# Performance work log

Measured on AMD Instinct MI355X. Metric: run time of the kernel, lower is better.

Reference implementation:

```python
import jax, jax.numpy as jnp
import numpy as np

N_NODES = 50000
N_EDGES = 400000
D_IN = 2048
D_OUT = 512


def setup_inputs() -> dict:
    key = jax.random.key(0)
    k1, k2, k3 = jax.random.split(key, 3)
    x = jax.random.normal(k1, (N_NODES, D_IN), dtype=jnp.float32)
    edge_index = jax.random.randint(k2, (2, N_EDGES), 0, N_NODES, dtype=jnp.int64)
    # Glorot init like PyG GCNConv
    scale = jnp.sqrt(6.0 / (D_IN + D_OUT)).astype(jnp.float32)
    weight = jax.random.uniform(k3, (D_IN, D_OUT), dtype=jnp.float32, minval=-scale, maxval=scale)
    bias = jnp.zeros((D_OUT,), dtype=jnp.float32)
    return {"x": x, "edge_index": edge_index, "weight": weight, "bias": bias}


def reference(x, edge_index, weight, bias):
    N = x.shape[0]
    # GCNConv(normalize=True): add self-loops, symmetric deg^-1/2 normalization
    loops = jnp.arange(N, dtype=edge_index.dtype)
    src = jnp.concatenate([edge_index[0], loops])  # message sources (x_j)
    dst = jnp.concatenate([edge_index[1], loops])  # aggregation targets
    ones = jnp.ones(dst.shape[0], dtype=x.dtype)
    deg = jax.ops.segment_sum(ones, dst, num_segments=N)  # [N]
    deg_inv_sqrt = jnp.where(deg > 0, jax.lax.rsqrt(deg), 0.0)
    norm = deg_inv_sqrt[src] * deg_inv_sqrt[dst]  # [E+N]
    h = x @ weight  # [N, d_out] linear transform before propagation
    msgs = norm[:, None] * h[src]  # [E+N, d_out]
    out = jax.ops.segment_sum(msgs, dst, num_segments=N) + bias  # [N, d_out]
    return jax.nn.log_softmax(out, axis=1)
```

## Files before the change

kernel.cpp:

```cpp
#include <hip/hip_runtime.h>
#include <stdint.h>

#define D_IN   2048
#define D_OUT  512

typedef __bf16 bf16;
typedef bf16     bf16x8 __attribute__((ext_vector_type(8)));
typedef float    f32x4  __attribute__((ext_vector_type(4)));
typedef uint32_t u32x4  __attribute__((ext_vector_type(4)));

#define GLP(p)  (const __attribute__((address_space(1))) void*)(p)
#define LDSP(p) (__attribute__((address_space(3))) void*)(p)

__global__ void k_count(const int* __restrict__ dstv, int* __restrict__ cnt, int E) {
    int e = blockIdx.x * blockDim.x + threadIdx.x;
    if (e < E) atomicAdd(&cnt[dstv[e]], 1);
}

__global__ __launch_bounds__(1024) void k_scan1(const int* __restrict__ cnt,
                                                int* __restrict__ offs,
                                                int* __restrict__ bsum,
                                                float* __restrict__ dis,
                                                int* __restrict__ cur, int n) {
    __shared__ int wsum[16], wbase[16];
    const int tid = threadIdx.x, lane = tid & 63, wv = tid >> 6;
    int i = blockIdx.x * 1024 + tid;
    int v = (i < n) ? cnt[i] : 0;
    int x = v;
    #pragma unroll
    for (int d = 1; d < 64; d <<= 1) {
        int y = __shfl_up(x, d);
        if (lane >= d) x += y;
    }
    if (lane == 63) wsum[wv] = x;
    __syncthreads();
    if (tid < 16) {
        int s = 0;
        for (int j = 0; j < tid; ++j) s += wsum[j];
        wbase[tid] = s;
    }
    __syncthreads();
    if (i < n) {
        offs[i] = wbase[wv] + x - v;
        dis[i]  = rsqrtf((float)(v + 1));
        cur[i]  = 0;
    }
    if (tid == 0) bsum[blockIdx.x] = wbase[15] + wsum[15];
}

__global__ void k_scan2(int* __restrict__ bsum, int nb) {
    int t = threadIdx.x;
    if (nb <= 64) {
        int v = (t < nb) ? bsum[t] : 0;
        int x = v;
        #pragma unroll
        for (int d = 1; d < 64; d <<= 1) {
            int y = __shfl_up(x, d);
            if (t >= d) x += y;
        }
        if (t < nb) bsum[t] = x - v;
    } else if (t == 0) {
        int run = 0;
        for (int j = 0; j < nb; ++j) { int v = bsum[j]; bsum[j] = run; run += v; }
    }
}

__global__ void k_fill(const int* __restrict__ srcv, const int* __restrict__ dstv,
                       const int* __restrict__ offs, const int* __restrict__ bsum,
                       int* __restrict__ cur, int* __restrict__ csr, int E) {
    int e = blockIdx.x * blockDim.x + threadIdx.x;
    if (e < E) {
        int d = dstv[e];
        int p = offs[d] + bsum[d >> 10] + atomicAdd(&cur[d], 1);
        csr[p] = srcv[e];
    }
}

__global__ void k_wt(const float* __restrict__ W, uint16_t* __restrict__ wt) {
    __shared__ float t[32][33];
    int kb = blockIdx.x * 32, nb = blockIdx.y * 32;
    int tx = threadIdx.x, ty = threadIdx.y;
    #pragma unroll
    for (int i = 0; i < 32; i += 8)
        t[ty + i][tx] = W[(size_t)(kb + ty + i) * D_OUT + nb + tx];
    __syncthreads();
    bf16* o = (bf16*)wt;
    #pragma unroll
    for (int i = 0; i < 32; i += 8)
        o[(size_t)(nb + ty + i) * D_IN + kb + tx] = (bf16)t[tx][ty + i];
}

__global__ __launch_bounds__(256) void k_gemm(const float* __restrict__ X,
                                              const uint16_t* __restrict__ WT,
                                              uint16_t* __restrict__ H, int M) {
    __shared__ uint16_t lsA[128 * 64];
    __shared__ uint16_t lsB[128 * 64];
    const int nwg = gridDim.x;
    const int b = blockIdx.x;
    const int q = nwg >> 3, r = nwg & 7;
    const int xcd = b & 7, lo = b >> 3;
    const int g = (xcd < r) ? (xcd * (q + 1) + lo) : (r * (q + 1) + (xcd - r) * q + lo);
    const int m0 = (g >> 2) * 128;
    const int n0 = (g & 3) * 128;
    const int tid = threadIdx.x;
    const int w = tid >> 6, lane = tid & 63;
    const int wr = w >> 1, wc = w & 1;
    const int lr = lane & 15, lk = lane >> 4;

    f32x4 acc[4][4];
    #pragma unroll
    for (int m = 0; m < 4; m++)
        #pragma unroll
        for (int n = 0; n < 4; n++) acc[m][n] = (f32x4)(0.0f);

    const float* aSrc[4];
    int aDst[4];
    const uint16_t* bSrc[4];
    #pragma unroll
    for (int j = 0; j < 4; j++) {
        int uidx = (w * 4 + j) * 64 + lane;
        int row = uidx >> 3, u = uidx & 7;
        int lrow = row;
        if (m0 + row >= M) lrow = (M - 1) - m0;
        aSrc[j] = X + (size_t)(m0 + lrow) * D_IN + u * 8;
        aDst[j] = row * 64 + (u ^ (row & 7)) * 8;
        bSrc[j] = WT + (size_t)(n0 + row) * D_IN + (u ^ (row & 7)) * 8;
    }

    for (int k0 = 0; k0 < D_IN; k0 += 64) {
        #pragma unroll
        for (int j = 0; j < 4; j++)
            __builtin_amdgcn_global_load_lds(GLP(bSrc[j] + k0),
                                             LDSP(lsB + (w * 4 + j) * 512), 16, 0, 0);
        #pragma unroll
        for (int j = 0; j < 4; j++) {
            f32x4 a0 = *(const f32x4*)(aSrc[j] + k0);
            f32x4 a1 = *(const f32x4*)(aSrc[j] + k0 + 4);
            bf16x8 t;
            t[0] = (bf16)a0[0]; t[1] = (bf16)a0[1]; t[2] = (bf16)a0[2]; t[3] = (bf16)a0[3];
            t[4] = (bf16)a1[0]; t[5] = (bf16)a1[1]; t[6] = (bf16)a1[2]; t[7] = (bf16)a1[3];
            *(bf16x8*)(lsA + aDst[j]) = t;
        }
        __syncthreads();

        #pragma unroll
        for (int kk = 0; kk < 2; kk++) {
            bf16x8 aF[4], bF[4];
            #pragma unroll
            for (int m = 0; m < 4; m++) {
                int row = wr * 64 + m * 16 + lr;
                aF[m] = *(const bf16x8*)(lsA + row * 64 + (((kk * 4 + lk) ^ (row & 7)) * 8));
            }
            #pragma unroll
            for (int n = 0; n < 4; n++) {
                int row = wc * 64 + n * 16 + lr;
                bF[n] = *(const bf16x8*)(lsB + row * 64 + (((kk * 4 + lk) ^ (row & 7)) * 8));
            }
            #pragma unroll
            for (int m = 0; m < 4; m++)
                #pragma unroll
                for (int n = 0; n < 4; n++)
                    acc[m][n] = __builtin_amdgcn_mfma_f32_16x16x32_bf16(aF[m], bF[n], acc[m][n], 0, 0, 0);
        }
        __syncthreads();
    }

    #pragma unroll
    for (int m = 0; m < 4; m++) {
        int rbase = m0 + wr * 64 + m * 16 + lk * 4;
        #pragma unroll
        for (int n = 0; n < 4; n++) {
            int col = n0 + wc * 64 + n * 16 + lr;
            #pragma unroll
            for (int j = 0; j < 4; j++) {
                int row = rbase + j;
                if (row < M) {
                    bf16 t = (bf16)acc[m][n][j];
                    H[(size_t)row * D_OUT + col] = __builtin_bit_cast(uint16_t, t);
                }
            }
        }
    }
}

__global__ __launch_bounds__(256) void k_agg(const uint16_t* __restrict__ h,
                                             const int* __restrict__ csr,
                                             const int* __restrict__ offs,
                                             const int* __restrict__ bsum,
                                             const int* __restrict__ cnt,
                                             const float* __restrict__ dis,
                                             const float* __restrict__ bias,
                                             float* __restrict__ out, int N) {
    const int wv = threadIdx.x >> 6, lane = threadIdx.x & 63;
    const int i = blockIdx.x * 4 + wv;
    if (i >= N) return;
    const float di = dis[i];
    float acc[8];
    {
        u32x4 v = *(const u32x4*)(h + (size_t)i * D_OUT + lane * 8);
        float s2 = di * di;
        #pragma unroll
        for (int k = 0; k < 4; k++) {
            acc[2 * k]     = __builtin_bit_cast(float, v[k] << 16) * s2;
            acc[2 * k + 1] = __builtin_bit_cast(float, v[k] & 0xffff0000u) * s2;
        }
    }
    const int o = offs[i] + bsum[i >> 10], c = cnt[i];
    for (int e = o; e < o + c; ++e) {
        int s = csr[e];
        float ws = di * dis[s];
        u32x4 v = *(const u32x4*)(h + (size_t)s * D_OUT + lane * 8);
        #pragma unroll
        for (int k = 0; k < 4; k++) {
            acc[2 * k]     += __builtin_bit_cast(float, v[k] << 16) * ws;
            acc[2 * k + 1] += __builtin_bit_cast(float, v[k] & 0xffff0000u) * ws;
        }
    }
    {
        const f32x4* bp = (const f32x4*)(bias + lane * 8);
        f32x4 b0 = bp[0], b1 = bp[1];
        #pragma unroll
        for (int k = 0; k < 4; k++) { acc[k] += b0[k]; acc[4 + k] += b1[k]; }
    }
    float mx = acc[0];
    #pragma unroll
    for (int k = 1; k < 8; k++) mx = fmaxf(mx, acc[k]);
    #pragma unroll
    for (int d = 1; d < 64; d <<= 1) mx = fmaxf(mx, __shfl_xor(mx, d));
    float se = 0.f;
    #pragma unroll
    for (int k = 0; k < 8; k++) se += expf(acc[k] - mx);
    #pragma unroll
    for (int d = 1; d < 64; d <<= 1) se += __shfl_xor(se, d);
    float lse = mx + logf(se);
    f32x4 o0, o1;
    #pragma unroll
    for (int k = 0; k < 4; k++) { o0[k] = acc[k] - lse; o1[k] = acc[4 + k] - lse; }
    f32x4* op = (f32x4*)(out + (size_t)i * D_OUT + lane * 8);
    op[0] = o0; op[1] = o1;
}

extern "C" void kernel_launch(void* const* d_in, const int* in_sizes, int n_in,
                              void* d_out, int out_size, void* d_ws, size_t ws_size,
                              hipStream_t stream) {
    const float* x    = (const float*)d_in[0];
    const int*   ei   = (const int*)d_in[1];
    const float* W    = (const float*)d_in[2];
    const float* bias = (const float*)d_in[3];
    float* out = (float*)d_out;

    const int N = in_sizes[0] / D_IN;
    const int E = in_sizes[1] / 2;
    const int* srcv = ei;
    const int* dstv = ei + E;

    char* p = (char*)d_ws;
    auto carve = [&](size_t b) { void* r = (void*)p; p += (b + 255) & ~(size_t)255; return r; };
    uint16_t* h    = (uint16_t*)carve((size_t)N * D_OUT * 2);
    uint16_t* wt   = (uint16_t*)carve((size_t)D_OUT * D_IN * 2);
    int*      cnt  = (int*)carve((size_t)N * 4);
    int*      cur  = (int*)carve((size_t)N * 4);
    float*    dis  = (float*)carve((size_t)N * 4);
    int*      offs = (int*)carve((size_t)N * 4);
    int*      csr  = (int*)carve((size_t)E * 4);
    int*      bsum = (int*)carve(1024 * 4);

    hipMemsetAsync(cnt, 0, (size_t)N * 4, stream);

    k_wt<<<dim3(D_IN / 32, D_OUT / 32), dim3(32, 8), 0, stream>>>(W, wt);
    k_count<<<(E + 255) / 256, 256, 0, stream>>>(dstv, cnt, E);
    const int nb = (N + 1023) / 1024;
    k_scan1<<<nb, 1024, 0, stream>>>(cnt, offs, bsum, dis, cur, N);
    k_scan2<<<1, 64, 0, stream>>>(bsum, nb);
    k_fill<<<(E + 255) / 256, 256, 0, stream>>>(srcv, dstv, offs, bsum, cur, csr, E);

    k_gemm<<<((N + 127) / 128) * 4, 256, 0, stream>>>(x, wt, h, N);

    k_agg<<<(N + 3) / 4, 256, 0, stream>>>(h, csr, offs, bsum, cnt, dis, bias, out, N);
}
```

Before: 369.1 us.

## Double-buffer GEMM LDS tiles and prefetch A into registers two steps ahead

Converts the bf16 GEMM main loop into a software pipeline. LDS A/B tiles are now double-buffered, and the next tile's B is staged asynchronously into LDS while the current tile computes. A's fp32 data is prefetched into registers two iterations ahead, which cuts the barrier count per iteration from two to one. The cost is double the LDS use (64KB per block), which may lower occupancy, plus more live registers.

```diff
diff --git a/kernel.cpp b/kernel.cpp
--- a/kernel.cpp
+++ b/kernel.cpp
@@ -93,8 +93,8 @@
 __global__ __launch_bounds__(256) void k_gemm(const float* __restrict__ X,
                                               const uint16_t* __restrict__ WT,
                                               uint16_t* __restrict__ H, int M) {
-    __shared__ uint16_t lsA[128 * 64];
-    __shared__ uint16_t lsB[128 * 64];
+    __shared__ uint16_t lsA[2][128 * 64];
+    __shared__ uint16_t lsB[2][128 * 64];
     const int nwg = gridDim.x;
     const int b = blockIdx.x;
     const int q = nwg >> 3, r = nwg & 7;
@@ -106,6 +106,7 @@
     const int w = tid >> 6, lane = tid & 63;
     const int wr = w >> 1, wc = w & 1;
     const int lr = lane & 15, lk = lane >> 4;
+    const int NT = D_IN / 64;
 
     f32x4 acc[4][4];
     #pragma unroll
@@ -127,34 +128,45 @@
         bSrc[j] = WT + (size_t)(n0 + row) * D_IN + (u ^ (row & 7)) * 8;
     }
 
-    for (int k0 = 0; k0 < D_IN; k0 += 64) {
+    f32x4 ar0[4], ar1[4];
+
+    auto loadA = [&](int t) {
+        #pragma unroll
+        for (int j = 0; j < 4; j++) {
+            ar0[j] = *(const f32x4*)(aSrc[j] + t * 64);
+            ar1[j] = *(const f32x4*)(aSrc[j] + t * 64 + 4);
+        }
+    };
+    auto writeA = [&](int buf) {
+        #pragma unroll
+        for (int j = 0; j < 4; j++) {
+            bf16x8 tv;
+            tv[0] = (bf16)ar0[j][0]; tv[1] = (bf16)ar0[j][1];
+            tv[2] = (bf16)ar0[j][2]; tv[3] = (bf16)ar0[j][3];
+            tv[4] = (bf16)ar1[j][0]; tv[5] = (bf16)ar1[j][1];
+            tv[6] = (bf16)ar1[j][2]; tv[7] = (bf16)ar1[j][3];
+            *(bf16x8*)(&lsA[buf][aDst[j]]) = tv;
+        }
+    };
+    auto stageB = [&](int t, int buf) {
         #pragma unroll
         for (int j = 0; j < 4; j++)
-            __builtin_amdgcn_global_load_lds(GLP(bSrc[j] + k0),
-                                             LDSP(lsB + (w * 4 + j) * 512), 16, 0, 0);
-        #pragma unroll
-        for (int j = 0; j < 4; j++) {
-            f32x4 a0 = *(const f32x4*)(aSrc[j] + k0);
-            f32x4 a1 = *(const f32x4*)(aSrc[j] + k0 + 4);
-            bf16x8 t;
-            t[0] = (bf16)a0[0]; t[1] = (bf16)a0[1]; t[2] = (bf16)a0[2]; t[3] = (bf16)a0[3];
-            t[4] = (bf16)a1[0]; t[5] = (bf16)a1[1]; t[6] = (bf16)a1[2]; t[7] = (bf16)a1[3];
-            *(bf16x8*)(lsA + aDst[j]) = t;
-        }
-        __syncthreads();
-
+            __builtin_amdgcn_global_load_lds(GLP(bSrc[j] + t * 64),
+                                             LDSP(&lsB[buf][(w * 4 + j) * 512]), 16, 0, 0);
+    };
+    auto compute = [&](int buf) {
         #pragma unroll
         for (int kk = 0; kk < 2; kk++) {
             bf16x8 aF[4], bF[4];
             #pragma unroll
             for (int m = 0; m < 4; m++) {
                 int row = wr * 64 + m * 16 + lr;
-                aF[m] = *(const bf16x8*)(lsA + row * 64 + (((kk * 4 + lk) ^ (row & 7)) * 8));
+                aF[m] = *(const bf16x8*)(&lsA[buf][row * 64 + (((kk * 4 + lk) ^ (row & 7)) * 8)]);
             }
             #pragma unroll
             for (int n = 0; n < 4; n++) {
                 int row = wc * 64 + n * 16 + lr;
-                bF[n] = *(const bf16x8*)(lsB + row * 64 + (((kk * 4 + lk) ^ (row & 7)) * 8));
+                bF[n] = *(const bf16x8*)(&lsB[buf][row * 64 + (((kk * 4 + lk) ^ (row & 7)) * 8)]);
             }
             #pragma unroll
             for (int m = 0; m < 4; m++)
@@ -162,7 +174,27 @@
                 for (int n = 0; n < 4; n++)
                     acc[m][n] = __builtin_amdgcn_mfma_f32_16x16x32_bf16(aF[m], bF[n], acc[m][n], 0, 0, 0);
         }
+    };
+    auto body = [&](int t, int bufc) {
+        int bufn = bufc ^ 1;
+        if (t + 1 < NT) {
+            stageB(t + 1, bufn);
+            writeA(bufn);
+            loadA(t + 2 < NT ? t + 2 : t);
+        }
+        compute(bufc);
         __syncthreads();
+    };
+
+    loadA(0);
+    stageB(0, 0);
+    writeA(0);
+    loadA(1);
+    __syncthreads();
+
+    for (int t = 0; t < NT; t += 2) {
+        body(t, 0);
+        body(t + 1, 1);
     }
 
     #pragma unroll
```

After: 480.0 us. +30.1%, slower.

## Double-buffer B tile in LDS and load A fragments directly from global

Applied to the files above, without the earlier changes.

The GEMM no longer stages the fp32 X tile through LDS. Each wave reads its A fragments straight from global memory and converts them to bf16 in registers. The B tile is double-buffered in LDS so the async load of the next tile overlaps the MFMA work on the current one, and launch bounds now request 3 workgroups per CU. The aim is to cut LDS traffic and barrier stalls. In exchange, each 128-column block reads A from global redundantly across the two column-waves (wc), which leans on cache hits, and the occupancy hint may force register spills.

```diff
diff --git a/kernel.cpp b/kernel.cpp
--- a/kernel.cpp
+++ b/kernel.cpp
@@ -90,11 +90,10 @@
         o[(size_t)(nb + ty + i) * D_IN + kb + tx] = (bf16)t[tx][ty + i];
 }
 
-__global__ __launch_bounds__(256) void k_gemm(const float* __restrict__ X,
-                                              const uint16_t* __restrict__ WT,
-                                              uint16_t* __restrict__ H, int M) {
-    __shared__ uint16_t lsA[128 * 64];
-    __shared__ uint16_t lsB[128 * 64];
+__global__ __launch_bounds__(256, 3) void k_gemm(const float* __restrict__ X,
+                                                 const uint16_t* __restrict__ WT,
+                                                 uint16_t* __restrict__ H, int M) {
+    __shared__ uint16_t lsB[2][128 * 64];
     const int nwg = gridDim.x;
     const int b = blockIdx.x;
     const int q = nwg >> 3, r = nwg & 7;
@@ -106,6 +105,7 @@
     const int w = tid >> 6, lane = tid & 63;
     const int wr = w >> 1, wc = w & 1;
     const int lr = lane & 15, lk = lane >> 4;
+    const int NT = D_IN / 64;
 
     f32x4 acc[4][4];
     #pragma unroll
@@ -113,48 +113,46 @@
         #pragma unroll
         for (int n = 0; n < 4; n++) acc[m][n] = (f32x4)(0.0f);
 
-    const float* aSrc[4];
-    int aDst[4];
+    const float* aRow[4];
+    #pragma unroll
+    for (int m = 0; m < 4; m++) {
+        int row = m0 + wr * 64 + m * 16 + lr;
+        if (row >= M) row = M - 1;
+        aRow[m] = X + (size_t)row * D_IN + lk * 8;
+    }
+
     const uint16_t* bSrc[4];
     #pragma unroll
     for (int j = 0; j < 4; j++) {
         int uidx = (w * 4 + j) * 64 + lane;
         int row = uidx >> 3, u = uidx & 7;
-        int lrow = row;
-        if (m0 + row >= M) lrow = (M - 1) - m0;
-        aSrc[j] = X + (size_t)(m0 + lrow) * D_IN + u * 8;
-        aDst[j] = row * 64 + (u ^ (row & 7)) * 8;
         bSrc[j] = WT + (size_t)(n0 + row) * D_IN + (u ^ (row & 7)) * 8;
     }
 
-    for (int k0 = 0; k0 < D_IN; k0 += 64) {
+    auto stageB = [&](int t, int buf) {
         #pragma unroll
         for (int j = 0; j < 4; j++)
-            __builtin_amdgcn_global_load_lds(GLP(bSrc[j] + k0),
-                                             LDSP(lsB + (w * 4 + j) * 512), 16, 0, 0);
-        #pragma unroll
-        for (int j = 0; j < 4; j++) {
-            f32x4 a0 = *(const f32x4*)(aSrc[j] + k0);
-            f32x4 a1 = *(const f32x4*)(aSrc[j] + k0 + 4);
-            bf16x8 t;
-            t[0] = (bf16)a0[0]; t[1] = (bf16)a0[1]; t[2] = (bf16)a0[2]; t[3] = (bf16)a0[3];
-            t[4] = (bf16)a1[0]; t[5] = (bf16)a1[1]; t[6] = (bf16)a1[2]; t[7] = (bf16)a1[3];
-            *(bf16x8*)(lsA + aDst[j]) = t;
-        }
-        __syncthreads();
-
+            __builtin_amdgcn_global_load_lds(GLP(bSrc[j] + t * 64),
+                                             LDSP(&lsB[buf][(w * 4 + j) * 512]), 16, 0, 0);
+    };
+    auto compute = [&](int t, int buf) {
         #pragma unroll
         for (int kk = 0; kk < 2; kk++) {
             bf16x8 aF[4], bF[4];
             #pragma unroll
             for (int m = 0; m < 4; m++) {
-                int row = wr * 64 + m * 16 + lr;
-                aF[m] = *(const bf16x8*)(lsA + row * 64 + (((kk * 4 + lk) ^ (row & 7)) * 8));
+                const float* ap = aRow[m] + t * 64 + kk * 32;
+                f32x4 a0 = *(const f32x4*)ap;
+                f32x4 a1 = *(const f32x4*)(ap + 4);
+                bf16x8 tv;
+                tv[0] = (bf16)a0[0]; tv[1] = (bf16)a0[1]; tv[2] = (bf16)a0[2]; tv[3] = (bf16)a0[3];
+                tv[4] = (bf16)a1[0]; tv[5] = (bf16)a1[1]; tv[6] = (bf16)a1[2]; tv[7] = (bf16)a1[3];
+                aF[m] = tv;
             }
             #pragma unroll
             for (int n = 0; n < 4; n++) {
                 int row = wc * 64 + n * 16 + lr;
-                bF[n] = *(const bf16x8*)(lsB + row * 64 + (((kk * 4 + lk) ^ (row & 7)) * 8));
+                bF[n] = *(const bf16x8*)(&lsB[buf][row * 64 + (((kk * 4 + lk) ^ (row & 7)) * 8)]);
             }
             #pragma unroll
             for (int m = 0; m < 4; m++)
@@ -162,6 +160,16 @@
                 for (int n = 0; n < 4; n++)
                     acc[m][n] = __builtin_amdgcn_mfma_f32_16x16x32_bf16(aF[m], bF[n], acc[m][n], 0, 0, 0);
         }
+    };
+
+    stageB(0, 0);
+    __syncthreads();
+    for (int t = 0; t < NT; t += 2) {
+        if (t + 1 < NT) stageB(t + 1, 1);
+        compute(t, 0);
+        __syncthreads();
+        if (t + 2 < NT) stageB(t + 2, 0);
+        compute(t + 1, 1);
         __syncthreads();
     }
 
@@ -175,8 +183,8 @@
             for (int j = 0; j < 4; j++) {
                 int row = rbase + j;
                 if (row < M) {
-                    bf16 t = (bf16)acc[m][n][j];
-                    H[(size_t)row * D_OUT + col] = __builtin_bit_cast(uint16_t, t);
+                    bf16 tv = (bf16)acc[m][n][j];
+                    H[(size_t)row * D_OUT + col] = __builtin_bit_cast(uint16_t, tv);
                 }
             }
         }
```

New measurement: 660.4 us. 1.79x slower.
